# Optimization experiments

Measured on AMD Instinct MI355X. Metric: run time of the kernel, lower is better.

Reference implementation:

```python
import jax, jax.numpy as jnp
import numpy as np

B, S, D, H = 2, 2048, 1024, 16
HD = D // H  # head_dim = 64


def setup_inputs() -> dict:
    key = jax.random.key(0)
    ks = jax.random.split(key, 7)
    s = 0.02
    return {
        "queries": jax.random.normal(ks[0], (B, S, D), jnp.float32),
        "keys": jax.random.normal(ks[1], (B, S, D), jnp.float32),
        "values": jax.random.normal(ks[2], (B, S, D), jnp.float32),
        "Wq": jax.random.normal(ks[3], (D, D), jnp.float32) * s,
        "Wk": jax.random.normal(ks[4], (D, D), jnp.float32) * s,
        "Wv": jax.random.normal(ks[5], (D, D), jnp.float32) * s,
        "Wo": jax.random.normal(ks[6], (D, D), jnp.float32) * s,
    }


def reference(queries, keys, values, Wq, Wk, Wv, Wo):
    # Projections (torch Linear: x @ W.T); split into heads -> [B, H, S, HD]
    def split_heads(x):
        b, s, _ = x.shape
        return x.reshape(b, s, H, HD).transpose(0, 2, 1, 3)

    q = split_heads(queries @ Wq.T)
    k = split_heads(keys @ Wk.T)
    v = split_heads(values @ Wv.T)

    scale = 1.0 / jnp.sqrt(jnp.asarray(HD, q.dtype))
    scores = jnp.einsum("bhqd,bhkd->bhqk", q, k) * scale  # [B,H,S,S]
    attn = jax.nn.softmax(scores, axis=-1)
    ctx = jnp.einsum("bhqk,bhkd->bhqd", attn, v)  # [B,H,S,HD]
    out = ctx.transpose(0, 2, 1, 3).reshape(queries.shape[0], -1, D)
    return out @ Wo.T
```

## Files before the change

### kernel.cpp

```cpp
#include <hip/hip_runtime.h>
#include <hip/hip_bf16.h>


#define B_ 2
#define S_ 2048
#define D_ 1024
#define H_ 16
#define HD_ 64
#define NE_ (B_ * S_ * D_)
#define WN_ (D_ * D_)

typedef unsigned short u16;
typedef unsigned int u32;
typedef u16 __attribute__((may_alias)) u16_ma;
typedef float __attribute__((may_alias)) f32_ma;
typedef u32 v4u __attribute__((ext_vector_type(4)));
typedef v4u __attribute__((may_alias)) v4u_ma;
typedef short bf16x8 __attribute__((ext_vector_type(8)));
typedef bf16x8 __attribute__((may_alias)) bf16x8_ma;
typedef float f32x4 __attribute__((ext_vector_type(4)));
typedef float f32x16 __attribute__((ext_vector_type(16)));

__device__ __forceinline__ float bf2f(u16 u) {
  u32 x = ((u32)u) << 16;
  return __builtin_bit_cast(float, x);
}
__device__ __forceinline__ u16 f2bf(float f) {
  __hip_bfloat16 h = __float2bfloat16(f);
  return __builtin_bit_cast(u16, h);
}
__device__ __forceinline__ u16 rne1(float f) {
  u32 a = __builtin_bit_cast(u32, f);
  a += 0x7FFFu + ((a >> 16) & 1u);
  return (u16)(a >> 16);
}
__device__ __forceinline__ u32 rne_pair(float lo, float hi) {
  u32 a = __builtin_bit_cast(u32, lo);
  u32 b = __builtin_bit_cast(u32, hi);
  a += 0x7FFFu + ((a >> 16) & 1u);
  b += 0x7FFFu + ((b >> 16) & 1u);
  return (a >> 16) | (b & 0xFFFF0000u);
}
__device__ __forceinline__ u32 pk2(u32 alo, u32 ahi) {
  return (u32)f2bf(__builtin_bit_cast(float, alo)) |
         ((u32)f2bf(__builtin_bit_cast(float, ahi)) << 16);
}

__device__ __forceinline__ void gl_lds16(const void* g, u16* l) {
  auto gp = (const __attribute__((address_space(1))) unsigned int*)g;
  auto lp = (__attribute__((address_space(3))) unsigned int*)(void*)l;
  __builtin_amdgcn_global_load_lds(gp, lp, 16, 0, 0);
}

__device__ __forceinline__ bool detect_f32(const u16* Wg) {
  const int lane = threadIdx.x & 63;
  bool hit = false;
#pragma unroll
  for (int i = 0; i < 4; ++i) {
    v4u u = *(const v4u_ma*)(Wg + lane * 32 + i * 8);
#pragma unroll
    for (int j = 0; j < 4; ++j) {
      u32 w = u[j];
      hit |= (((w >> 7) & 0xFFu) >= 0xF0u) || (((w >> 23) & 0xFFu) >= 0xF0u);
    }
  }
  return __any(hit);
}

__global__ __launch_bounds__(256) void convert_bf16(
    const void* s0, const void* s1, const void* s2, const void* s3,
    const void* s4, const void* s5, const void* s6, u16* __restrict__ dst_in,
    u16* __restrict__ dst_w, const u16* __restrict__ Wdet, int mode) {
  const bool det = (mode == 1) ? true : detect_f32(Wdet);
  if (!det) return;
  const int y = blockIdx.y;
  const void* src;
  u16* dst;
  int n;
  if (y < 3) {
    src = (y == 0) ? s0 : ((y == 1) ? s1 : s2);
    dst = dst_in + (size_t)y * NE_;
    n = NE_;
  } else {
    src = (y == 3) ? s3 : ((y == 4) ? s4 : ((y == 5) ? s5 : s6));
    dst = dst_w + (size_t)(y - 3) * WN_;
    n = WN_;
  }
  const int i = (blockIdx.x * 256 + threadIdx.x) * 8;
  if (i >= n) return;
  const v4u_ma* fp = (const v4u_ma*)((const float*)src + i);
  v4u f0 = fp[0], f1 = fp[1];
  v4u out;
  out[0] = pk2(f0[0], f0[1]);
  out[1] = pk2(f0[2], f0[3]);
  out[2] = pk2(f1[0], f1[1]);
  out[3] = pk2(f1[2], f1[3]);
  *(v4u_ma*)(dst + i) = out;
}

template <int BN, bool OUT_DET>
__global__ __launch_bounds__(256) void proj_g(
    const u16* __restrict__ Asc, const u16* __restrict__ Wsc,
    void* __restrict__ Cb, const u16* __restrict__ Wdet,
    const u16* __restrict__ Ao0, const u16* __restrict__ Ao1,
    const u16* __restrict__ Ao2, const u16* __restrict__ Wo0,
    const u16* __restrict__ Wo1, const u16* __restrict__ Wo2, int mode) {
  __shared__ u16 Al[2][128 * 32];
  __shared__ u16 Wl[2][BN * 32];

  const bool det = (mode == 1) ? true : ((mode == 0) ? false : detect_f32(Wdet));
  const int z = blockIdx.z;

  const u16* Aptr;
  const u16* Wptr;
  if (OUT_DET) {
    Aptr = Asc;
    Wptr = det ? Wsc : Wo0;
  } else {
    Aptr = det ? (Asc + (size_t)z * NE_)
               : (z == 0 ? Ao0 : (z == 1 ? Ao1 : Ao2));
    Wptr = det ? (Wsc + (size_t)z * WN_)
               : (z == 0 ? Wo0 : (z == 1 ? Wo1 : Wo2));
  }

  const int tid = threadIdx.x;
  const int lane = tid & 63, wid = tid >> 6;
  const int lg = lane >> 4, li = lane & 15;
  const int wr = wid >> 1, wc = wid & 1;
  const int m0 = blockIdx.x * 128, n0 = blockIdx.y * BN;

  const int srow = lane >> 2;
  const int scol = (lane & 3) * 8;

  auto issue = [&](int bi, int kt) {
    const int k0 = kt * 32;
#pragma unroll
    for (int c = 0; c < 2; ++c) {
      const int rbase = c * 64 + wid * 16;
      gl_lds16(Aptr + (size_t)(m0 + rbase + srow) * D_ + k0 + scol,
               &Al[bi][rbase * 32]);
    }
    if constexpr (BN == 128) {
#pragma unroll
      for (int c = 0; c < 2; ++c) {
        const int rbase = c * 64 + wid * 16;
        gl_lds16(Wptr + (size_t)(n0 + rbase + srow) * D_ + k0 + scol,
                 &Wl[bi][rbase * 32]);
      }
    } else {
      const int rbase = wid * 16;
      gl_lds16(Wptr + (size_t)(n0 + rbase + srow) * D_ + k0 + scol,
               &Wl[bi][rbase * 32]);
    }
  };

  constexpr int NF = BN / 32;
  f32x4 acc[4][NF];
#pragma unroll
  for (int m = 0; m < 4; ++m)
#pragma unroll
    for (int n = 0; n < NF; ++n) acc[m][n] = (f32x4){0.f, 0.f, 0.f, 0.f};

  issue(0, 0);

  for (int kt = 0; kt < 32; ++kt) {
    const int cur = kt & 1;
    if (kt < 31) {
      issue(cur ^ 1, kt + 1);
      if constexpr (BN == 128)
        asm volatile("s_waitcnt vmcnt(4)" ::: "memory");
      else
        asm volatile("s_waitcnt vmcnt(3)" ::: "memory");
    } else {
      asm volatile("s_waitcnt vmcnt(0)" ::: "memory");
    }
    __builtin_amdgcn_s_barrier();
    asm volatile("" ::: "memory");

    bf16x8 af[4], bw[NF];
#pragma unroll
    for (int m = 0; m < 4; ++m)
      af[m] = *(const bf16x8_ma*)(&Al[cur][(wr * 64 + m * 16 + li) * 32] + lg * 8);
#pragma unroll
    for (int n = 0; n < NF; ++n)
      bw[n] = *(const bf16x8_ma*)(&Wl[cur][(wc * (BN / 2) + n * 16 + li) * 32] +
                                  lg * 8);
#pragma unroll
    for (int m = 0; m < 4; ++m)
#pragma unroll
      for (int n = 0; n < NF; ++n)
        acc[m][n] = __builtin_amdgcn_mfma_f32_16x16x32_bf16(af[m], bw[n],
                                                            acc[m][n], 0, 0, 0);

    asm volatile("" ::: "memory");
    __builtin_amdgcn_s_barrier();
  }

  const bool outf32 = OUT_DET ? det : false;
  const float zs = (!OUT_DET && z == 0) ? 0.125f : 1.0f;
#pragma unroll
  for (int m = 0; m < 4; ++m)
#pragma unroll
    for (int n = 0; n < NF; ++n)
#pragma unroll
      for (int r = 0; r < 4; ++r) {
        const int row = m0 + wr * 64 + m * 16 + lg * 4 + r;
        const int col = n0 + wc * (BN / 2) + n * 16 + li;
        const size_t idx = (size_t)row * D_ + col;
        const float v = acc[m][n][r] * zs;
        if (OUT_DET) {
          if (outf32)
            ((f32_ma*)Cb)[idx] = v;
          else
            ((u16_ma*)Cb)[idx] = rne1(v);
        } else {
          ((u16_ma*)((u16*)Cb + (size_t)z * NE_))[idx] = rne1(v);
        }
      }
}

__global__ __launch_bounds__(256) void attn3(
    const u16* __restrict__ Qg, const u16* __restrict__ Kg,
    const u16* __restrict__ Vg, u16* __restrict__ Og) {
  __shared__ u16 Kl[2][64 * 64];
  __shared__ u16 VTl[2][64 * 64];

  const int tid = threadIdx.x;
  const int wid = tid >> 6, lane = tid & 63;
  const int l31 = lane & 31;
  const int hi = lane >> 5;

  const int bid = blockIdx.x;
  const int swz = (bid & 7) * 64 + (bid >> 3);
  const int qb = swz & 15;
  const int h = (swz >> 4) & 15;
  const int b = swz >> 8;
  const size_t bbase = (size_t)b * S_ * D_;
  const int hoff = h * HD_;
  const int q0w = qb * 128 + wid * 32;

  bf16x8 bq[4];
  {
    const u16* qp = Qg + bbase + (size_t)(q0w + l31) * D_ + hoff + hi * 8;
#pragma unroll
    for (int dblk = 0; dblk < 4; ++dblk)
      bq[dblk] = *(const bf16x8_ma*)(qp + dblk * 16);
  }

  f32x16 o0, o1;
#pragma unroll
  for (int i = 0; i < 16; ++i) {
    o0[i] = 0.f;
    o1[i] = 0.f;
  }
  float mrun = -1e30f, lrun = 0.f;

  const int lr8 = lane >> 3;
  const int ksz = ((lane & 7) * 16) ^ (lr8 << 4);
  auto k_dma = [&](int bi, int kt) {
    const int key0 = kt * 64;
#pragma unroll
    for (int p = 0; p < 2; ++p) {
      const int row0 = wid * 16 + p * 8;
      const u16* srow = Kg + bbase + (size_t)(key0 + row0 + lr8) * D_ + hoff;
      gl_lds16((const char*)srow + ksz, &Kl[bi][row0 * 64]);
    }
  };

  const int vkr = lane;
  const int vd0 = wid * 8;
  v4u vr0, vr1;
  auto v_load = [&](int kt) {
    const int key0 = kt * 64;
    vr0 = *(const v4u_ma*)(Vg + bbase + (size_t)(key0 + vkr) * D_ + hoff + vd0);
    vr1 = *(const v4u_ma*)(Vg + bbase + (size_t)(key0 + vkr) * D_ + hoff + vd0 + 32);
  };
  auto v_write = [&](int bi) {
    char* Vb = (char*)&VTl[bi][0];
    union {
      v4u v;
      u16 e[8];
    } uu;
    uu.v = vr0;
#pragma unroll
    for (int j = 0; j < 8; ++j) {
      const int d = vd0 + j;
      *(u16*)(Vb + d * 128 + ((vkr * 2) ^ ((d & 7) << 4))) = uu.e[j];
    }
    uu.v = vr1;
#pragma unroll
    for (int j = 0; j < 8; ++j) {
      const int d = vd0 + 32 + j;
      *(u16*)(Vb + d * 128 + ((vkr * 2) ^ ((d & 7) << 4))) = uu.e[j];
    }
  };

  k_dma(0, 0);
  v_load(0);
  asm volatile("s_waitcnt vmcnt(0)" ::: "memory");
  v_write(0);

  const int swk = (l31 & 7) << 4;

  for (int kt = 0; kt < S_ / 64; ++kt) {
    __syncthreads();
    const int cur = kt & 1;
    if (kt < S_ / 64 - 1) {
      k_dma(cur ^ 1, kt + 1);
      v_load(kt + 1);
    }

    const char* Kb = (const char*)&Kl[cur][0];
    const char* Vb = (const char*)&VTl[cur][0];

    f32x16 sT0, sT1;
#pragma unroll
    for (int i = 0; i < 16; ++i) {
      sT0[i] = 0.f;
      sT1[i] = 0.f;
    }
    __builtin_amdgcn_s_setprio(1);
#pragma unroll
    for (int dblk = 0; dblk < 4; ++dblk) {
      const int cb = (dblk * 32 + hi * 16);
      bf16x8 a0 = *(const bf16x8_ma*)(Kb + l31 * 128 + (cb ^ swk));
      bf16x8 a1 = *(const bf16x8_ma*)(Kb + (32 + l31) * 128 + (cb ^ swk));
      sT0 = __builtin_amdgcn_mfma_f32_32x32x16_bf16(a0, bq[dblk], sT0, 0, 0, 0);
      sT1 = __builtin_amdgcn_mfma_f32_32x32x16_bf16(a1, bq[dblk], sT1, 0, 0, 0);
    }
    __builtin_amdgcn_s_setprio(0);

    float t[16];
#pragma unroll
    for (int i = 0; i < 16; ++i) t[i] = fmaxf(sT0[i], sT1[i]);
#pragma unroll
    for (int s = 8; s; s >>= 1)
#pragma unroll
      for (int i = 0; i < s; ++i) t[i] = fmaxf(t[i], t[i + s]);
    float pmax = fmaxf(t[0], __shfl_xor(t[0], 32));
    if (!__all(pmax - mrun <= 8.0f)) {
      const float mnew = fmaxf(mrun, pmax);
      const float al = __expf(mrun - mnew);
      mrun = mnew;
      lrun *= al;
      o0 *= al;
      o1 *= al;
    }

    u32 w[16];
    float ps[16];
#pragma unroll
    for (int kh = 0; kh < 2; ++kh)
#pragma unroll
      for (int g = 0; g < 4; ++g)
#pragma unroll
        for (int u = 0; u < 2; ++u) {
          const int r = g * 4 + 2 * u;
          const float pe = __expf((kh ? sT1[r] : sT0[r]) - mrun);
          const float po = __expf((kh ? sT1[r + 1] : sT0[r + 1]) - mrun);
          ps[kh * 8 + g * 2 + u] = pe + po;
          w[kh * 8 + g * 2 + u] = rne_pair(pe, po);
        }
#pragma unroll
    for (int s = 8; s; s >>= 1)
#pragma unroll
      for (int i = 0; i < s; ++i) ps[i] += ps[i + s];
    lrun += ps[0] + __shfl_xor(ps[0], 32);

    bf16x8 pf[4];
#pragma unroll
    for (int km = 0; km < 4; ++km) {
      const int a = 4 * km;
      const u32 s0 = hi ? w[a] : w[a + 2];
      const u32 s1 = hi ? w[a + 1] : w[a + 3];
      const u32 r0 = (u32)__shfl_xor((int)s0, 32);
      const u32 r1 = (u32)__shfl_xor((int)s1, 32);
      union {
        u32 d[4];
        bf16x8 v;
      } uu;
      uu.d[0] = hi ? r0 : w[a];
      uu.d[1] = hi ? r1 : w[a + 1];
      uu.d[2] = hi ? w[a + 2] : r0;
      uu.d[3] = hi ? w[a + 3] : r1;
      pf[km] = uu.v;
    }

    __builtin_amdgcn_s_setprio(1);
#pragma unroll
    for (int km = 0; km < 4; ++km) {
      const int cb = (km * 32 + hi * 16);
      bf16x8 v0 = *(const bf16x8_ma*)(Vb + l31 * 128 + (cb ^ swk));
      bf16x8 v1 = *(const bf16x8_ma*)(Vb + (32 + l31) * 128 + (cb ^ swk));
      o0 = __builtin_amdgcn_mfma_f32_32x32x16_bf16(v0, pf[km], o0, 0, 0, 0);
      o1 = __builtin_amdgcn_mfma_f32_32x32x16_bf16(v1, pf[km], o1, 0, 0, 0);
    }
    __builtin_amdgcn_s_setprio(0);

    if (kt < S_ / 64 - 1) {
      asm volatile("s_waitcnt vmcnt(0)" ::: "memory");
      v_write(cur ^ 1);
    }
  }

  const float inv = 1.f / lrun;
  u16* orow = Og + bbase + (size_t)(q0w + l31) * D_ + hoff;
#pragma unroll
  for (int r = 0; r < 16; ++r) {
    const int d0 = (r & 3) + 8 * (r >> 2) + 4 * hi;
    orow[d0] = rne1(o0[r] * inv);
    orow[d0 + 32] = rne1(o1[r] * inv);
  }
}

template <bool A_SCR, bool SCR_F32, bool OUT_FINAL>
__global__ __launch_bounds__(256) void proj_slow(
    const void* __restrict__ Ag, const u16* __restrict__ Wg,
    void* __restrict__ Cg) {
  const bool det = detect_f32(Wg);
  const bool a_f32 = A_SCR ? SCR_F32 : det;
  const int m = blockIdx.x;
  const int n = blockIdx.y * 256 + threadIdx.x;
  const size_t arow = (size_t)m * D_;
  const size_t wrow = (size_t)n * D_;
  float acc = 0.f;
  for (int k = 0; k < D_; ++k) {
    float a = a_f32 ? ((const f32_ma*)Ag)[arow + k]
                    : bf2f(((const u16_ma*)Ag)[arow + k]);
    float w = det ? ((const f32_ma*)Wg)[wrow + k]
                  : bf2f(((const u16_ma*)Wg)[wrow + k]);
    acc += a * w;
  }
  const size_t ci = (size_t)m * D_ + n;
  const bool c_f32 = OUT_FINAL ? det : SCR_F32;
  if (c_f32)
    ((f32_ma*)Cg)[ci] = acc;
  else
    ((u16_ma*)Cg)[ci] = f2bf(acc);
}

template <bool SCR_F32>
__global__ __launch_bounds__(256) void attn_slow(
    const void* __restrict__ Qg, const void* __restrict__ Kg,
    const void* __restrict__ Vg, void* __restrict__ Cg) {
  const int tid = threadIdx.x;
  const int qblk = blockIdx.x & 7;
  const int h = (blockIdx.x >> 3) & 15;
  const int b = blockIdx.x >> 7;
  const int q = qblk * 256 + tid;
  const size_t base = (size_t)b * S_ * D_;
  const int hoff = h * HD_;
  float qv[64];
  {
    const size_t qrow = base + (size_t)q * D_ + hoff;
    for (int d = 0; d < 64; ++d)
      qv[d] = SCR_F32 ? ((const f32_ma*)Qg)[qrow + d]
                      : bf2f(((const u16_ma*)Qg)[qrow + d]);
  }
  float o[64];
  for (int d = 0; d < 64; ++d) o[d] = 0.f;
  float m = -1e30f, l = 0.f;
  for (int key = 0; key < S_; ++key) {
    const size_t krow = base + (size_t)key * D_ + hoff;
    float s = 0.f;
    for (int d = 0; d < 64; ++d) {
      float kx = SCR_F32 ? ((const f32_ma*)Kg)[krow + d]
                         : bf2f(((const u16_ma*)Kg)[krow + d]);
      s += qv[d] * kx;
    }
    s *= 0.125f;
    float mn = fmaxf(m, s);
    float al = expf(m - mn);
    float pe = expf(s - mn);
    m = mn;
    l = l * al + pe;
    for (int d = 0; d < 64; ++d) {
      float vx = SCR_F32 ? ((const f32_ma*)Vg)[krow + d]
                         : bf2f(((const u16_ma*)Vg)[krow + d]);
      o[d] = o[d] * al + pe * vx;
    }
  }
  const float il = 1.f / l;
  const size_t crow = base + (size_t)q * D_ + hoff;
  for (int d = 0; d < 64; ++d) {
    if (SCR_F32)
      ((f32_ma*)Cg)[crow + d] = o[d] * il;
    else
      ((u16_ma*)Cg)[crow + d] = f2bf(o[d] * il);
  }
}

extern "C" void kernel_launch(void* const* d_in, const int* in_sizes, int n_in,
                              void* d_out, int out_size, void* d_ws,
                              size_t ws_size, hipStream_t stream) {
  const u16* Wdet = (const u16*)d_in[3];
  dim3 blk(256);

  int mode = 2;
  if (n_in >= 7 && in_sizes) {
    if (in_sizes[0] == (int)((size_t)NE_ * 2)) mode = 0;
    else if (in_sizes[0] == (int)((size_t)NE_ * 4)) mode = 1;
  }

  if (ws_size >= (size_t)4 * NE_ * sizeof(float)) {
    u16* Qi = (u16*)d_ws;
    u16* Wc = Qi + (size_t)3 * NE_;
    u16* Qp = Wc + (size_t)4 * WN_;
    u16* Xp = Qp + (size_t)3 * NE_;

    if (mode != 0) {
      convert_bf16<<<dim3(2048, 7), blk, 0, stream>>>(
          d_in[0], d_in[1], d_in[2], d_in[3], d_in[4], d_in[5], d_in[6], Qi,
          Wc, Wdet, mode);
    }
    proj_g<128, false><<<dim3(32, 8, 3), blk, 0, stream>>>(
        Qi, Wc, Qp, Wdet, (const u16*)d_in[0], (const u16*)d_in[1],
        (const u16*)d_in[2], (const u16*)d_in[3], (const u16*)d_in[4],
        (const u16*)d_in[5], mode);
    attn3<<<dim3(512), blk, 0, stream>>>(Qp, Qp + NE_, Qp + (size_t)2 * NE_, Xp);
    proj_g<64, true><<<dim3(32, 16, 1), blk, 0, stream>>>(
        Xp, Wc + (size_t)3 * WN_, d_out, Wdet, nullptr, nullptr, nullptr,
        (const u16*)d_in[6], nullptr, nullptr, mode);
  } else {
    dim3 gproj(B_ * S_, D_ / 256);
    dim3 gattn(B_ * H_ * (S_ / 256));
    u16* Qp = (u16*)d_out;
    u16* Kp = (u16*)d_in[0];
    u16* Vp = (u16*)d_in[1];
    u16* Xp = (u16*)d_in[2];
    proj_slow<false, false, false><<<gproj, blk, 0, stream>>>(
        d_in[0], (const u16*)d_in[3], Qp);
    proj_slow<false, false, false><<<gproj, blk, 0, stream>>>(
        d_in[1], (const u16*)d_in[4], Kp);
    proj_slow<false, false, false><<<gproj, blk, 0, stream>>>(
        d_in[2], (const u16*)d_in[5], Vp);
    attn_slow<false><<<gattn, blk, 0, stream>>>(Qp, Kp, Vp, Xp);
    proj_slow<true, false, true><<<gproj, blk, 0, stream>>>(
        Xp, (const u16*)d_in[6], d_out);
  }
}
```

Before: 244.1 us.

## Split attention KV range in two and merge partials with log-sum-exp

In bf16-input mode the attention kernel now launches 1024 blocks, each covering half of the key sequence. Each block writes unnormalized fp32 partial outputs and per-row (max, sum) stats to workspace and to the output buffer. A new merge kernel then combines the two halves into bf16. The aim is more blocks to fill the GPU, at the cost of an extra kernel and extra fp32 traffic. The mode detection heuristic is also widened to check weight and output byte sizes.

```diff
diff --git a/kernel.cpp b/kernel.cpp
--- a/kernel.cpp
+++ b/kernel.cpp
@@ -219,9 +219,11 @@
       }
 }
 
-__global__ __launch_bounds__(256) void attn3(
+template <bool SPLIT2>
+__global__ __launch_bounds__(256) void attn3t(
     const u16* __restrict__ Qg, const u16* __restrict__ Kg,
-    const u16* __restrict__ Vg, u16* __restrict__ Og) {
+    const u16* __restrict__ Vg, u16* __restrict__ Og,
+    float* __restrict__ Po, float2* __restrict__ St) {
   __shared__ u16 Kl[2][64 * 64];
   __shared__ u16 VTl[2][64 * 64];
 
@@ -231,13 +233,22 @@
   const int hi = lane >> 5;
 
   const int bid = blockIdx.x;
-  const int swz = (bid & 7) * 64 + (bid >> 3);
-  const int qb = swz & 15;
-  const int h = (swz >> 4) & 15;
-  const int b = swz >> 8;
+  int split = 0, r9;
+  if constexpr (SPLIT2) {
+    const int swz = (bid & 7) * 128 + (bid >> 3);
+    split = swz >> 9;
+    r9 = swz & 511;
+  } else {
+    r9 = (bid & 7) * 64 + (bid >> 3);
+  }
+  const int qb = r9 & 15;
+  const int h = (r9 >> 4) & 15;
+  const int b = r9 >> 8;
   const size_t bbase = (size_t)b * S_ * D_;
   const int hoff = h * HD_;
   const int q0w = qb * 128 + wid * 32;
+  const int kt0 = SPLIT2 ? split * (S_ / 128) : 0;
+  const int ktN = SPLIT2 ? (S_ / 128) : (S_ / 64);
 
   bf16x8 bq[4];
   {
@@ -295,17 +306,18 @@
     }
   };
 
-  k_dma(0, 0);
-  v_load(0);
+  k_dma(0, kt0);
+  v_load(kt0);
   asm volatile("s_waitcnt vmcnt(0)" ::: "memory");
   v_write(0);
 
   const int swk = (l31 & 7) << 4;
 
-  for (int kt = 0; kt < S_ / 64; ++kt) {
+  for (int it = 0; it < ktN; ++it) {
+    const int kt = kt0 + it;
     __syncthreads();
-    const int cur = kt & 1;
-    if (kt < S_ / 64 - 1) {
+    const int cur = it & 1;
+    if (it < ktN - 1) {
       k_dma(cur ^ 1, kt + 1);
       v_load(kt + 1);
     }
@@ -397,20 +409,60 @@
     }
     __builtin_amdgcn_s_setprio(0);
 
-    if (kt < S_ / 64 - 1) {
+    if (it < ktN - 1) {
       asm volatile("s_waitcnt vmcnt(0)" ::: "memory");
       v_write(cur ^ 1);
     }
   }
 
-  const float inv = 1.f / lrun;
-  u16* orow = Og + bbase + (size_t)(q0w + l31) * D_ + hoff;
-#pragma unroll
-  for (int r = 0; r < 16; ++r) {
-    const int d0 = (r & 3) + 8 * (r >> 2) + 4 * hi;
-    orow[d0] = rne1(o0[r] * inv);
-    orow[d0 + 32] = rne1(o1[r] * inv);
-  }
+  if constexpr (SPLIT2) {
+    float* Pg = Po + (size_t)split * NE_ + bbase + (size_t)(q0w + l31) * D_ + hoff;
+#pragma unroll
+    for (int r = 0; r < 16; ++r) {
+      const int d0 = (r & 3) + 8 * (r >> 2) + 4 * hi;
+      Pg[d0] = o0[r];
+      Pg[d0 + 32] = o1[r];
+    }
+    if (!hi) {
+      const int sidx = (((b << 4) | h) << 11) | (q0w + l31);
+      St[(size_t)split * 65536 + sidx] = make_float2(mrun, lrun);
+    }
+  } else {
+    const float inv = 1.f / lrun;
+    u16* orow = Og + bbase + (size_t)(q0w + l31) * D_ + hoff;
+#pragma unroll
+    for (int r = 0; r < 16; ++r) {
+      const int d0 = (r & 3) + 8 * (r >> 2) + 4 * hi;
+      orow[d0] = rne1(o0[r] * inv);
+      orow[d0 + 32] = rne1(o1[r] * inv);
+    }
+  }
+}
+
+__global__ __launch_bounds__(256) void merge_splits(
+    const float* __restrict__ Po, const float2* __restrict__ St,
+    u16* __restrict__ Xp) {
+  const int i = (blockIdx.x * 256 + threadIdx.x) * 8;
+  const int row = i >> 10;
+  const int col = i & 1023;
+  const int b = row >> 11, q = row & 2047, h = col >> 6;
+  const int sidx = (((b << 4) | h) << 11) | q;
+  const float2 s1 = St[sidx];
+  const float2 s2 = St[65536 + sidx];
+  const float m = fmaxf(s1.x, s2.x);
+  float a1 = __expf(s1.x - m), a2 = __expf(s2.x - m);
+  const float inv = 1.f / (a1 * s1.y + a2 * s2.y);
+  a1 *= inv;
+  a2 *= inv;
+  const f32x4* O1 = (const f32x4*)(Po + i);
+  const f32x4* O2 = (const f32x4*)(Po + NE_ + i);
+  f32x4 x0 = O1[0], x1 = O1[1], y0 = O2[0], y1 = O2[1];
+  v4u out;
+  out[0] = rne_pair(a1 * x0[0] + a2 * y0[0], a1 * x0[1] + a2 * y0[1]);
+  out[1] = rne_pair(a1 * x0[2] + a2 * y0[2], a1 * x0[3] + a2 * y0[3]);
+  out[2] = rne_pair(a1 * x1[0] + a2 * y1[0], a1 * x1[1] + a2 * y1[1]);
+  out[3] = rne_pair(a1 * x1[2] + a2 * y1[2], a1 * x1[3] + a2 * y1[3]);
+  *(v4u_ma*)(Xp + i) = out;
 }
 
 template <bool A_SCR, bool SCR_F32, bool OUT_FINAL>
@@ -498,8 +550,11 @@
 
   int mode = 2;
   if (n_in >= 7 && in_sizes) {
-    if (in_sizes[0] == (int)((size_t)NE_ * 2)) mode = 0;
-    else if (in_sizes[0] == (int)((size_t)NE_ * 4)) mode = 1;
+    const bool bf16_bytes = (in_sizes[0] == 8388608) ||
+                            (in_sizes[3] == 2097152) || (out_size == 8388608);
+    const bool f32_bytes = (in_sizes[0] == 16777216) || (out_size == 16777216);
+    if (bf16_bytes) mode = 0;
+    else if (f32_bytes) mode = 1;
   }
 
   if (ws_size >= (size_t)4 * NE_ * sizeof(float)) {
@@ -517,7 +572,16 @@
         Qi, Wc, Qp, Wdet, (const u16*)d_in[0], (const u16*)d_in[1],
         (const u16*)d_in[2], (const u16*)d_in[3], (const u16*)d_in[4],
         (const u16*)d_in[5], mode);
-    attn3<<<dim3(512), blk, 0, stream>>>(Qp, Qp + NE_, Qp + (size_t)2 * NE_, Xp);
+    if (mode == 0) {
+      float* Po = (float*)d_ws;
+      float2* St = (float2*)d_out;
+      attn3t<true><<<dim3(1024), blk, 0, stream>>>(
+          Qp, Qp + NE_, Qp + (size_t)2 * NE_, nullptr, Po, St);
+      merge_splits<<<dim3(2048), blk, 0, stream>>>(Po, St, Xp);
+    } else {
+      attn3t<false><<<dim3(512), blk, 0, stream>>>(
+          Qp, Qp + NE_, Qp + (size_t)2 * NE_, Xp, nullptr, nullptr);
+    }
     proj_g<64, true><<<dim3(32, 16, 1), blk, 0, stream>>>(
         Xp, Wc + (size_t)3 * WN_, d_out, Wdet, nullptr, nullptr, nullptr,
         (const u16*)d_in[6], nullptr, nullptr, mode);
```

After: 245.2 us. No clear change (+0.4%).
